# Kernel optimization log

Measured on AMD Instinct MI355X. Metric: run time of the kernel, lower is better.

The kernel has to match this reference:

```python
import jax, jax.numpy as jnp
import numpy as np

B, D, NT, H, K = 4096, 112, 200, 512, 10
HID = 512
IN = 3 * D + NT + 1   # GRU input size = 537
M0 = H + 3 * D + NT   # MLP first-layer input = 1048


def setup_inputs() -> dict:
    key = jax.random.key(0)
    ks = jax.random.split(key, 9)
    def w(k, shape, fan):
        return jax.random.normal(k, shape, jnp.float32) / np.sqrt(fan).astype(np.float32)
    return {
        "z": jax.random.normal(ks[0], (B, D), jnp.float32),
        "c": jax.random.normal(ks[1], (B, D + NT), jnp.float32),
        "b": jax.random.uniform(ks[2], (B, D), jnp.float32),
        "m": jax.random.uniform(ks[3], (B, D), jnp.float32),
        "Wih": w(ks[4], (IN, 3 * H), IN),
        "Whh": w(ks[5], (H, 3 * H), H),
        "bih": jnp.zeros((3 * H,), jnp.float32),
        "bhh": jnp.zeros((3 * H,), jnp.float32),
        "W0": w(ks[6], (M0, HID), M0),
        "b0": jnp.zeros((HID,), jnp.float32),
        "W1": w(ks[7], (HID, HID), HID),
        "b1": jnp.zeros((HID,), jnp.float32),
        "W2": w(ks[8], (HID, 3 * K), HID),
        "b2": jnp.zeros((3 * K,), jnp.float32),
    }


def reference(z, c, b, m, Wih, Whh, bih, bhh, W0, b0, W1, b1, W2, b2):
    """AutoReg.logp: autoregressive GRU + MLP mixture-density head, gaussian base."""
    Bn = z.shape[0]
    const = jnp.concatenate([c, b, m], axis=1)          # [B, 3D+NT] fixed per step
    gi_const = const @ Wih[1:] + bih                    # input-proj of constant part
    w_z = Wih[0]                                        # [3H] weight for scalar z_t
    mlp_const = const @ W0[H:] + b0                     # const part of first MLP layer
    W0h = W0[:H]
    # teacher-forced previous-z sequence: z_0 = -1, then z[:, t-1]
    z_prev = jnp.concatenate([-jnp.ones((Bn, 1), z.dtype), z[:, :-1]], axis=1).T  # [D, B]

    def step(h, zt):  # h: [B,H], zt: [B]
        gi = zt[:, None] * w_z + gi_const               # [B, 3H]
        gh = h @ Whh + bhh
        ir, iz, inn = jnp.split(gi, 3, axis=1)
        hr, hz, hn = jnp.split(gh, 3, axis=1)
        r = jax.nn.sigmoid(ir + hr)
        u = jax.nn.sigmoid(iz + hz)
        n = jnp.tanh(inn + r * hn)
        h2 = (1.0 - u) * n + u * h                      # torch GRU update
        a = jnp.tanh(h2 @ W0h + mlp_const)              # Linear + Tanh on [h||c||b||m]
        a = jnp.tanh(a @ W1 + b1)
        p = a @ W2 + b2                                 # [B, 3K] mixture params
        return h2, p

    h0 = jnp.zeros((Bn, H), z.dtype)
    _, ps = jax.lax.scan(step, h0, z_prev)              # ps: [D, B, 3K]
    params = jnp.transpose(ps, (1, 0, 2))               # [B, D, 3K]

    logits, means, lsig = jnp.split(params, 3, axis=-1)
    sig = jnp.exp(lsig)
    t = z[..., None]
    log_norm = -lsig - 0.5 * np.float32(np.log(2.0 * np.pi))
    log_kern = -0.5 * jnp.square((t - means) / sig)
    ll = jax.nn.logsumexp(log_kern + log_norm + logits, axis=-1) \
         - jax.nn.logsumexp(logits, axis=-1)            # [B, D]

    query = m * (1.0 - b)
    mask = -jnp.sort(-query, axis=1)                    # descending sort values
    return jnp.sum(ll * mask, axis=1)                   # [B]
```

## Files before the change

kernel.cpp:

```cpp
#include <hip/hip_runtime.h>
#include <hip/hip_bf16.h>
#include <float.h>
#include <math.h>

#define BN   4096
#define DD   112
#define HH   512
#define G3   1536
#define CW   536
#define CWP  544
#define HIDD 512

typedef __attribute__((ext_vector_type(8))) short short8;
typedef __attribute__((ext_vector_type(4))) float float4v;

__device__ __forceinline__ unsigned short f2bf(float x) {
    __hip_bfloat16 h = __float2bfloat16(x);
    return *(unsigned short*)&h;
}
__device__ __forceinline__ unsigned char f2fp8(float x) {
    int v = __builtin_amdgcn_cvt_pk_fp8_f32(x, x, 0, false);
    return (unsigned char)(v & 0xff);
}

__global__ void build_constbf(const float* __restrict__ c, const float* __restrict__ b,
                              const float* __restrict__ m, unsigned short* __restrict__ out) {
    int idx = blockIdx.x * blockDim.x + threadIdx.x;
    if (idx >= BN * CWP) return;
    int row = idx / CWP, col = idx - row * CWP;
    float v;
    if (col < 312)      v = c[row * 312 + col];
    else if (col < 424) v = b[row * 112 + (col - 312)];
    else if (col < 536) v = m[row * 112 + (col - 424)];
    else                v = 0.0f;
    out[idx] = f2bf(v);
}

__global__ void zero_f32(float* __restrict__ p, int n) {
    int i = blockIdx.x * blockDim.x + threadIdx.x;
    if (i < n) p[i] = 0.0f;
}

__global__ void pack_wN(const float* __restrict__ src, unsigned short* __restrict__ dst,
                        int kchunks, int ldn, int ncols, int nrows) {
    int bid = blockIdx.x;
    int nt = bid / kchunks, kc = bid - nt * kchunks;
    int lane = threadIdx.x;
    int quad = lane >> 4, l16 = lane & 15;
    int n = nt * 16 + l16;
    unsigned short v[8];
#pragma unroll
    for (int j = 0; j < 8; ++j) {
        int k = kc * 32 + quad * 8 + j;
        float f = (k < nrows && n < ncols) ? src[(size_t)k * ldn + n] : 0.0f;
        v[j] = f2bf(f);
    }
    unsigned short* p = dst + ((size_t)bid * 64 + lane) * 8;
#pragma unroll
    for (int j = 0; j < 8; ++j) p[j] = v[j];
}

__global__ void pack_w8(const float* __restrict__ src, unsigned char* __restrict__ dst,
                        int kchunks, int ldn) {
    int bid = blockIdx.x;
    int nt = bid / kchunks, kc = bid - nt * kchunks;
    int lane = threadIdx.x;
    int quad = lane >> 4, l16 = lane & 15;
    int n = nt * 16 + l16;
    unsigned char v[8];
#pragma unroll
    for (int j = 0; j < 8; ++j) {
        int k = kc * 32 + quad * 8 + j;
        v[j] = f2fp8(src[(size_t)k * ldn + n]);
    }
    unsigned char* p = dst + ((size_t)bid * 64 + lane) * 8;
#pragma unroll
    for (int j = 0; j < 8; ++j) p[j] = v[j];
}

template<int TPW>
__global__ __launch_bounds__(1024) void gemm_const_mfma(
    const unsigned short* __restrict__ A, const unsigned short* __restrict__ BP,
    const float* __restrict__ bias, float* __restrict__ C, int N)
{
    const int tid = threadIdx.x;
    const int wave = tid >> 6, lane = tid & 63;
    const int quad = lane >> 4, l16 = lane & 15;
    const int rowBase = blockIdx.x * 16;
    const short8* BF = (const short8*)BP;
    float4v acc[TPW];
#pragma unroll
    for (int i = 0; i < TPW; ++i) {
        float bv = bias[(wave + 16 * i) * 16 + l16];
        acc[i] = (float4v){bv, bv, bv, bv};
    }
#pragma unroll 4
    for (int kc = 0; kc < 17; ++kc) {
        short8 af = *(const short8*)&A[(size_t)(rowBase + l16) * CWP + kc * 32 + quad * 8];
#pragma unroll
        for (int i = 0; i < TPW; ++i) {
            int tile = wave + 16 * i;
            acc[i] = __builtin_amdgcn_mfma_f32_16x16x32_bf16(af, BF[(tile * 17 + kc) * 64 + lane], acc[i], 0, 0, 0);
        }
    }
#pragma unroll
    for (int i = 0; i < TPW; ++i) {
        int col = (wave + 16 * i) * 16 + l16;
#pragma unroll
        for (int rg = 0; rg < 4; ++rg)
            C[(size_t)(rowBase + quad * 4 + rg) * N + col] = acc[i][rg];
    }
}

__global__ void sort_mask(const float* __restrict__ b, const float* __restrict__ m,
                          float* __restrict__ maskbuf) {
    __shared__ float s[128];
    const int row = blockIdx.x, t = threadIdx.x;
    float v = -FLT_MAX;
    if (t < DD) v = m[row * DD + t] * (1.0f - b[row * DD + t]);
    s[t] = v;
    __syncthreads();
    for (int k = 2; k <= 128; k <<= 1) {
        for (int j = k >> 1; j > 0; j >>= 1) {
            int ixj = t ^ j;
            if (ixj > t) {
                bool up = ((t & k) == 0);
                float a = s[t], bb = s[ixj];
                if ((a > bb) == up) { s[t] = bb; s[ixj] = a; }
            }
            __syncthreads();
        }
    }
    if (t < DD) maskbuf[row * DD + t] = s[127 - t];
}

__global__ __launch_bounds__(1024, 4) void gru_rec_chunk(
    const float* __restrict__ z, const float* __restrict__ Wih,
    const float* __restrict__ bhh, const float* __restrict__ gi_const,
    const unsigned short* __restrict__ WhhP, const unsigned char* __restrict__ Whh8P,
    float* __restrict__ hstate, unsigned short* __restrict__ h2g,
    int t0, int tlen)
{
    __shared__ unsigned short h_bf[2][16 * 520];
    __shared__ unsigned char h8[2][16 * 528];
    __shared__ float zbuf[113 * 16];

    const int tid = threadIdx.x;
    const int wave = tid >> 6, lane = tid & 63;
    const int quad = lane >> 4, l16 = lane & 15;
    const int rowBase = blockIdx.x * 16;

    for (int idx = tid; idx < 113 * 16; idx += 1024) {
        int tt = idx >> 4, r = idx & 15;
        zbuf[idx] = (tt == 0) ? -1.0f : z[(rowBase + r) * DD + tt - 1];
    }

    int hcol[2];
    float wz0[2], wz1[2], wz2[2], bh2r[2];
    float gic0[2][4], gic1[2][4], gic2[2][4];
    float h_own[2][4];
#pragma unroll
    for (int i = 0; i < 2; ++i) {
        int tile = wave + 16 * i;
        int hc = tile * 16 + l16;
        hcol[i] = hc;
        wz0[i] = Wih[hc]; wz1[i] = Wih[512 + hc]; wz2[i] = Wih[1024 + hc];
        float bh0 = bhh[hc], bh1 = bhh[512 + hc];
        bh2r[i] = bhh[1024 + hc];
#pragma unroll
        for (int rg = 0; rg < 4; ++rg) {
            int m = quad * 4 + rg;
            const float* g = gi_const + (size_t)(rowBase + m) * G3;
            gic0[i][rg] = g[hc] + bh0;
            gic1[i][rg] = g[512 + hc] + bh1;
            gic2[i][rg] = g[1024 + hc];
            float hv = hstate[(size_t)(rowBase + m) * HH + hc];
            h_own[i][rg] = hv;
            h_bf[0][m * 520 + hc] = f2bf(hv);
            h8[0][m * 528 + hc] = f2fp8(hv);
        }
    }
    const short8* WhhF = (const short8*)WhhP;
    const long* WhhF8 = (const long*)Whh8P;
    __syncthreads();

    for (int tt = 0; tt < tlen; ++tt) {
        const int t = t0 + tt;
        const int p = tt & 1;
        const unsigned short* hsrc = h_bf[p];
        const unsigned char* h8src = h8[p];
        unsigned short* hdst = h_bf[p ^ 1];
        unsigned char* h8dst = h8[p ^ 1];
        float4v accR[2], accU[2], accN[2];
#pragma unroll
        for (int i = 0; i < 2; ++i) {
            accR[i] = (float4v){gic0[i][0], gic0[i][1], gic0[i][2], gic0[i][3]};
            accU[i] = (float4v){gic1[i][0], gic1[i][1], gic1[i][2], gic1[i][3]};
            accN[i] = (float4v){0.f, 0.f, 0.f, 0.f};
        }
#pragma unroll 8
        for (int kc = 0; kc < 16; ++kc) {
            short8 af = *(const short8*)&hsrc[l16 * 520 + kc * 32 + quad * 8];
            long af8 = *(const long*)&h8src[l16 * 528 + kc * 32 + quad * 8];
#pragma unroll
            for (int i = 0; i < 2; ++i) {
                int tile = wave + 16 * i;
                accR[i] = __builtin_amdgcn_mfma_f32_16x16x32_fp8_fp8(af8, WhhF8[(tile * 16 + kc) * 64 + lane], accR[i], 0, 0, 0);
                accU[i] = __builtin_amdgcn_mfma_f32_16x16x32_fp8_fp8(af8, WhhF8[((tile + 32) * 16 + kc) * 64 + lane], accU[i], 0, 0, 0);
                accN[i] = __builtin_amdgcn_mfma_f32_16x16x32_bf16(af, WhhF[((tile + 64) * 16 + kc) * 64 + lane], accN[i], 0, 0, 0);
            }
        }
#pragma unroll
        for (int i = 0; i < 2; ++i) {
#pragma unroll
            for (int rg = 0; rg < 4; ++rg) {
                int m = quad * 4 + rg;
                float zt = zbuf[t * 16 + m];
                float r = 1.0f / (1.0f + __expf(-(accR[i][rg] + zt * wz0[i])));
                float u = 1.0f / (1.0f + __expf(-(accU[i][rg] + zt * wz1[i])));
                float xn = gic2[i][rg] + zt * wz2[i] + r * (accN[i][rg] + bh2r[i]);
                float n = 1.0f - 2.0f / (__expf(2.0f * xn) + 1.0f);
                float h2 = (1.0f - u) * n + u * h_own[i][rg];
                h_own[i][rg] = h2;
                hdst[m * 520 + hcol[i]] = f2bf(h2);
                h8dst[m * 528 + hcol[i]] = f2fp8(h2);
            }
        }
        __syncthreads();
        {
            int col = lane * 8;
            uint4 v = *(const uint4*)&hdst[wave * 520 + col];
            *(uint4*)&h2g[((size_t)tt * BN + rowBase + wave) * 512 + col] = v;
        }
    }
#pragma unroll
    for (int i = 0; i < 2; ++i)
#pragma unroll
        for (int rg = 0; rg < 4; ++rg)
            hstate[(size_t)(rowBase + quad * 4 + rg) * HH + hcol[i]] = h_own[i][rg];
}

__global__ __launch_bounds__(1024) void head_mdn64(
    const float* __restrict__ z, const float* __restrict__ b1,
    const float* __restrict__ b2, const float* __restrict__ mlp_const,
    const float* __restrict__ maskbuf, const unsigned short* __restrict__ h2g,
    const unsigned short* __restrict__ W0hP, const unsigned short* __restrict__ W1P,
    const unsigned short* __restrict__ W2P, float* __restrict__ out, int t0)
{
    __shared__ unsigned short h_bf[64 * 520];
    __shared__ unsigned short a_bf[64 * 520];
    float* ppf = (float*)a_bf;

    const int tid = threadIdx.x;
    const int wave = tid >> 6, lane = tid & 63;
    const int quad = lane >> 4, l16 = lane & 15;
    const int pr = tid >> 5, pc = tid & 31;
    const int b0 = blockIdx.x * 4;
    const int tg = blockIdx.y;
    const int phase = blockIdx.x & 15;

    {
        int flat = tid * 32;
        int r = flat >> 9, col = flat & 511;
        int bb = b0 + (r >> 4), trel = tg * 16 + (r & 15);
        const uint4* src = (const uint4*)&h2g[((size_t)trel * BN + bb) * 512 + col];
        uint4 v0 = src[0], v1 = src[1], v2 = src[2], v3 = src[3];
        uint4* dst = (uint4*)&h_bf[r * 520 + col];
        dst[0] = v0; dst[1] = v1; dst[2] = v2; dst[3] = v3;
    }
    int hcol[2];
    float b1c[2], mlc[2][4];
#pragma unroll
    for (int i = 0; i < 2; ++i) {
        int hc = (wave + 16 * i) * 16 + l16;
        hcol[i] = hc;
        b1c[i] = b1[hc];
#pragma unroll
        for (int mt = 0; mt < 4; ++mt) mlc[i][mt] = mlp_const[(size_t)(b0 + mt) * HIDD + hc];
    }
    const float b2v = (pc < 30) ? b2[pc] : 0.0f;
    const short8* W0hF = (const short8*)W0hP;
    const short8* W1F  = (const short8*)W1P;
    const short8* W2F  = (const short8*)W2P;
    __syncthreads();

    float4v acc1[2][4];
#pragma unroll
    for (int i = 0; i < 2; ++i)
#pragma unroll
        for (int mt = 0; mt < 4; ++mt)
            acc1[i][mt] = (float4v){mlc[i][mt], mlc[i][mt], mlc[i][mt], mlc[i][mt]};
#pragma unroll 2
    for (int kk = 0; kk < 16; ++kk) {
        const int kc = (kk + phase) & 15;
        short8 af[4];
#pragma unroll
        for (int mt = 0; mt < 4; ++mt)
            af[mt] = *(const short8*)&h_bf[(mt * 16 + l16) * 520 + kc * 32 + quad * 8];
#pragma unroll
        for (int i = 0; i < 2; ++i) {
            short8 bf = W0hF[((wave + 16 * i) * 16 + kc) * 64 + lane];
#pragma unroll
            for (int mt = 0; mt < 4; ++mt)
                acc1[i][mt] = __builtin_amdgcn_mfma_f32_16x16x32_bf16(af[mt], bf, acc1[i][mt], 0, 0, 0);
        }
    }
#pragma unroll
    for (int i = 0; i < 2; ++i)
#pragma unroll
        for (int mt = 0; mt < 4; ++mt)
#pragma unroll
            for (int rg = 0; rg < 4; ++rg) {
                int m = mt * 16 + quad * 4 + rg;
                float x = acc1[i][mt][rg];
                a_bf[m * 520 + hcol[i]] = f2bf(1.0f - 2.0f / (__expf(2.0f * x) + 1.0f));
            }
    __syncthreads();
    float4v acc2[2][4];
#pragma unroll
    for (int i = 0; i < 2; ++i)
#pragma unroll
        for (int mt = 0; mt < 4; ++mt)
            acc2[i][mt] = (float4v){b1c[i], b1c[i], b1c[i], b1c[i]};
#pragma unroll 2
    for (int kk = 0; kk < 16; ++kk) {
        const int kc = (kk + phase) & 15;
        short8 af[4];
#pragma unroll
        for (int mt = 0; mt < 4; ++mt)
            af[mt] = *(const short8*)&a_bf[(mt * 16 + l16) * 520 + kc * 32 + quad * 8];
#pragma unroll
        for (int i = 0; i < 2; ++i) {
            short8 bf = W1F[((wave + 16 * i) * 16 + kc) * 64 + lane];
#pragma unroll
            for (int mt = 0; mt < 4; ++mt)
                acc2[i][mt] = __builtin_amdgcn_mfma_f32_16x16x32_bf16(af[mt], bf, acc2[i][mt], 0, 0, 0);
        }
    }
    __syncthreads();
#pragma unroll
    for (int i = 0; i < 2; ++i)
#pragma unroll
        for (int mt = 0; mt < 4; ++mt)
#pragma unroll
            for (int rg = 0; rg < 4; ++rg) {
                int m = mt * 16 + quad * 4 + rg;
                float x = acc2[i][mt][rg];
                h_bf[m * 520 + hcol[i]] = f2bf(1.0f - 2.0f / (__expf(2.0f * x) + 1.0f));
            }
    __syncthreads();
    {
        const int mtw = wave >> 2, kg = wave & 3;
        float4v ap0 = (float4v){0.f, 0.f, 0.f, 0.f}, ap1 = (float4v){0.f, 0.f, 0.f, 0.f};
#pragma unroll
        for (int kk = 0; kk < 4; ++kk) {
            int kc = kg * 4 + kk;
            short8 af = *(const short8*)&h_bf[(mtw * 16 + l16) * 520 + kc * 32 + quad * 8];
            ap0 = __builtin_amdgcn_mfma_f32_16x16x32_bf16(af, W2F[(0 * 16 + kc) * 64 + lane], ap0, 0, 0, 0);
            ap1 = __builtin_amdgcn_mfma_f32_16x16x32_bf16(af, W2F[(1 * 16 + kc) * 64 + lane], ap1, 0, 0, 0);
        }
#pragma unroll
        for (int rg = 0; rg < 4; ++rg) {
            ppf[((kg * 4 + mtw) * 2 + 0) * 256 + lane * 4 + rg] = ap0[rg];
            ppf[((kg * 4 + mtw) * 2 + 1) * 256 + lane * 4 + rg] = ap1[rg];
        }
    }
    __syncthreads();
    float llm[2];
#pragma unroll
    for (int rh = 0; rh < 2; ++rh) {
        const int slot = rh * 32 + pr;
        const int bsub = slot >> 4, toff = slot & 15;
        const int mm = slot & 15;
        const int lane_c = ((mm >> 2) * 16 + (pc & 15));
        const int rgc = mm & 3, ntv = pc >> 4;
        float pv = b2v;
#pragma unroll
        for (int kg = 0; kg < 4; ++kg)
            pv += ppf[((kg * 4 + bsub) * 2 + ntv) * 256 + lane_c * 4 + rgc];
        const int half = lane & 32;
        float meanv = __shfl(pv, half + ((pc + 10) & 31), 64);
        float lsigv = __shfl(pv, half + ((pc + 20) & 31), 64);
        float e1, e2;
        if (pc < 10) {
            float ztar = z[(size_t)(b0 + bsub) * DD + t0 + tg * 16 + toff];
            float invs = __expf(-lsigv);
            float dd = (ztar - meanv) * invs;
            e1 = -0.5f * dd * dd - lsigv - 0.91893853320467274f + pv;
            e2 = pv;
        } else { e1 = -FLT_MAX; e2 = -FLT_MAX; }
        float m1 = e1, m2 = e2;
#pragma unroll
        for (int off = 16; off > 0; off >>= 1) {
            m1 = fmaxf(m1, __shfl_xor(m1, off, 64));
            m2 = fmaxf(m2, __shfl_xor(m2, off, 64));
        }
        float s1 = (pc < 10) ? __expf(e1 - m1) : 0.0f;
        float s2 = (pc < 10) ? __expf(e2 - m2) : 0.0f;
#pragma unroll
        for (int off = 16; off > 0; off >>= 1) {
            s1 += __shfl_xor(s1, off, 64);
            s2 += __shfl_xor(s2, off, 64);
        }
        float ll = (m1 + __logf(s1)) - (m2 + __logf(s2));
        llm[rh] = ll * maskbuf[(size_t)(b0 + bsub) * DD + t0 + tg * 16 + toff];
    }
    __syncthreads();
    if (pc == 0) { ppf[pr] = llm[0]; ppf[32 + pr] = llm[1]; }
    __syncthreads();
    if (tid < 4) {
        float s = 0.0f;
#pragma unroll
        for (int j = 0; j < 16; ++j) s += ppf[tid * 16 + j];
        atomicAdd(&out[b0 + tid], s);
    }
}

extern "C" void kernel_launch(void* const* d_in, const int* in_sizes, int n_in,
                              void* d_out, int out_size, void* d_ws, size_t ws_size,
                              hipStream_t stream) {
    const float* z   = (const float*)d_in[0];
    const float* c   = (const float*)d_in[1];
    const float* b   = (const float*)d_in[2];
    const float* m   = (const float*)d_in[3];
    const float* Wih = (const float*)d_in[4];
    const float* Whh = (const float*)d_in[5];
    const float* bih = (const float*)d_in[6];
    const float* bhh = (const float*)d_in[7];
    const float* W0  = (const float*)d_in[8];
    const float* b0  = (const float*)d_in[9];
    const float* W1  = (const float*)d_in[10];
    const float* b1  = (const float*)d_in[11];
    const float* W2  = (const float*)d_in[12];
    const float* b2  = (const float*)d_in[13];
    float* out = (float*)d_out;

    char* p = (char*)d_ws;
    unsigned short* constbf = (unsigned short*)p;  p += (size_t)BN * CWP * 2;
    float* gi_const  = (float*)p;                  p += (size_t)BN * G3 * 4;
    float* mlp_const = (float*)p;                  p += (size_t)BN * HIDD * 4;
    float* maskbuf   = (float*)p;                  p += (size_t)BN * DD * 4;
    unsigned short* WihP = (unsigned short*)p;     p += (size_t)96 * 17 * 512 * 2;
    unsigned short* W0cP = (unsigned short*)p;     p += (size_t)32 * 17 * 512 * 2;
    unsigned short* WhhP = (unsigned short*)p;     p += (size_t)96 * 16 * 512 * 2;
    unsigned short* W0hP = (unsigned short*)p;     p += (size_t)32 * 16 * 512 * 2;
    unsigned short* W1P  = (unsigned short*)p;     p += (size_t)32 * 16 * 512 * 2;
    unsigned short* W2P  = (unsigned short*)p;     p += (size_t)2 * 16 * 512 * 2;
    unsigned char* Whh8P = (unsigned char*)p;      p += (size_t)64 * 16 * 512;
    float* hstate        = (float*)p;              p += (size_t)BN * HH * 4;
    unsigned short* h2g  = (unsigned short*)p;

    const size_t base = (size_t)(p - (char*)d_ws);
    const size_t slab_per_t = (size_t)BN * 512 * 2;
    int TC = 0;
    if (ws_size > base) {
        TC = (int)((ws_size - base) / slab_per_t);
        TC = (TC / 16) * 16;
        if (TC > DD) TC = DD;
    }
    if (TC < 16) return;

    build_constbf<<<(BN * CWP + 255) / 256, 256, 0, stream>>>(c, b, m, constbf);
    pack_wN<<<96 * 17, 64, 0, stream>>>(Wih + G3, WihP, 17, G3, G3, CW);
    pack_wN<<<32 * 17, 64, 0, stream>>>(W0 + (size_t)HH * HIDD, W0cP, 17, HIDD, HIDD, CW);
    pack_wN<<<96 * 16, 64, 0, stream>>>(Whh, WhhP, 16, G3, G3, HH);
    pack_w8<<<64 * 16, 64, 0, stream>>>(Whh, Whh8P, 16, G3);
    pack_wN<<<32 * 16, 64, 0, stream>>>(W0,  W0hP, 16, HIDD, HIDD, HH);
    pack_wN<<<32 * 16, 64, 0, stream>>>(W1,  W1P,  16, HIDD, HIDD, HH);
    pack_wN<<<2 * 16, 64, 0, stream>>>(W2,  W2P,  16, 30, 30, HH);
    gemm_const_mfma<6><<<BN / 16, 1024, 0, stream>>>(constbf, WihP, bih, gi_const, G3);
    gemm_const_mfma<2><<<BN / 16, 1024, 0, stream>>>(constbf, W0cP, b0, mlp_const, HIDD);
    sort_mask<<<BN, 128, 0, stream>>>(b, m, maskbuf);

    zero_f32<<<(BN * HH + 255) / 256, 256, 0, stream>>>(hstate, BN * HH);
    zero_f32<<<(BN + 255) / 256, 256, 0, stream>>>(out, BN);
    for (int t0 = 0; t0 < DD; t0 += TC) {
        int tlen = DD - t0 < TC ? DD - t0 : TC;
        gru_rec_chunk<<<BN / 16, 1024, 0, stream>>>(z, Wih, bhh, gi_const, WhhP, Whh8P,
                                                    hstate, h2g, t0, tlen);
        dim3 gh(BN / 4, tlen / 16);
        head_mdn64<<<gh, 1024, 0, stream>>>(z, b1, b2, mlp_const, maskbuf, h2g,
                                            W0hP, W1P, W2P, out, t0);
    }
}
```

Measured before the change: 2.760 ms.

## Use FP8 for the GRU n-gate recurrent matmul and pair K-chunks into 16-byte loads

```diff
diff --git a/kernel.cpp b/kernel.cpp
--- a/kernel.cpp
+++ b/kernel.cpp
@@ -13,6 +13,7 @@
 
 typedef __attribute__((ext_vector_type(8))) short short8;
 typedef __attribute__((ext_vector_type(4))) float float4v;
+typedef __attribute__((ext_vector_type(2))) long long2v;
 
 __device__ __forceinline__ unsigned short f2bf(float x) {
     __hip_bfloat16 h = __float2bfloat16(x);
@@ -60,22 +61,22 @@
     for (int j = 0; j < 8; ++j) p[j] = v[j];
 }
 
-__global__ void pack_w8(const float* __restrict__ src, unsigned char* __restrict__ dst,
-                        int kchunks, int ldn) {
+__global__ void pack_w8p(const float* __restrict__ src, unsigned char* __restrict__ dst,
+                         int ldn) {
     int bid = blockIdx.x;
-    int nt = bid / kchunks, kc = bid - nt * kchunks;
+    int nt = bid >> 3, kp = bid & 7;
     int lane = threadIdx.x;
     int quad = lane >> 4, l16 = lane & 15;
     int n = nt * 16 + l16;
-    unsigned char v[8];
-#pragma unroll
-    for (int j = 0; j < 8; ++j) {
-        int k = kc * 32 + quad * 8 + j;
-        v[j] = f2fp8(src[(size_t)k * ldn + n]);
-    }
-    unsigned char* p = dst + ((size_t)bid * 64 + lane) * 8;
-#pragma unroll
-    for (int j = 0; j < 8; ++j) p[j] = v[j];
+    unsigned char v[16];
+#pragma unroll
+    for (int j2 = 0; j2 < 16; ++j2) {
+        int k = kp * 64 + (j2 >> 3) * 32 + quad * 8 + (j2 & 7);
+        v[j2] = f2fp8(src[(size_t)k * ldn + n]);
+    }
+    unsigned char* p = dst + ((size_t)bid * 64 + lane) * 16;
+#pragma unroll
+    for (int j2 = 0; j2 < 16; ++j2) p[j2] = v[j2];
 }
 
 template<int TPW>
@@ -137,7 +138,7 @@
 __global__ __launch_bounds__(1024, 4) void gru_rec_chunk(
     const float* __restrict__ z, const float* __restrict__ Wih,
     const float* __restrict__ bhh, const float* __restrict__ gi_const,
-    const unsigned short* __restrict__ WhhP, const unsigned char* __restrict__ Whh8P,
+    const unsigned char* __restrict__ Whh8P,
     float* __restrict__ hstate, unsigned short* __restrict__ h2g,
     int t0, int tlen)
 {
@@ -155,7 +156,7 @@
         zbuf[idx] = (tt == 0) ? -1.0f : z[(rowBase + r) * DD + tt - 1];
     }
 
-    int hcol[2];
+    int hcol[2], h8off[2];
     float wz0[2], wz1[2], wz2[2], bh2r[2];
     float gic0[2][4], gic1[2][4], gic2[2][4];
     float h_own[2][4];
@@ -164,6 +165,10 @@
         int tile = wave + 16 * i;
         int hc = tile * 16 + l16;
         hcol[i] = hc;
+        {
+            int kp = hc >> 6, rem = hc & 63;
+            h8off[i] = kp * 64 + ((rem & 31) >> 3) * 16 + (rem >> 5) * 8 + (rem & 7);
+        }
         wz0[i] = Wih[hc]; wz1[i] = Wih[512 + hc]; wz2[i] = Wih[1024 + hc];
         float bh0 = bhh[hc], bh1 = bhh[512 + hc];
         bh2r[i] = bhh[1024 + hc];
@@ -177,17 +182,15 @@
             float hv = hstate[(size_t)(rowBase + m) * HH + hc];
             h_own[i][rg] = hv;
             h_bf[0][m * 520 + hc] = f2bf(hv);
-            h8[0][m * 528 + hc] = f2fp8(hv);
-        }
-    }
-    const short8* WhhF = (const short8*)WhhP;
-    const long* WhhF8 = (const long*)Whh8P;
+            h8[0][m * 528 + h8off[i]] = f2fp8(hv);
+        }
+    }
+    const long2v* W8F = (const long2v*)Whh8P;
     __syncthreads();
 
     for (int tt = 0; tt < tlen; ++tt) {
         const int t = t0 + tt;
         const int p = tt & 1;
-        const unsigned short* hsrc = h_bf[p];
         const unsigned char* h8src = h8[p];
         unsigned short* hdst = h_bf[p ^ 1];
         unsigned char* h8dst = h8[p ^ 1];
@@ -199,15 +202,20 @@
             accN[i] = (float4v){0.f, 0.f, 0.f, 0.f};
         }
 #pragma unroll 8
-        for (int kc = 0; kc < 16; ++kc) {
-            short8 af = *(const short8*)&hsrc[l16 * 520 + kc * 32 + quad * 8];
-            long af8 = *(const long*)&h8src[l16 * 528 + kc * 32 + quad * 8];
+        for (int kp = 0; kp < 8; ++kp) {
+            long2v afp = *(const long2v*)&h8src[l16 * 528 + kp * 64 + quad * 16];
 #pragma unroll
             for (int i = 0; i < 2; ++i) {
                 int tile = wave + 16 * i;
-                accR[i] = __builtin_amdgcn_mfma_f32_16x16x32_fp8_fp8(af8, WhhF8[(tile * 16 + kc) * 64 + lane], accR[i], 0, 0, 0);
-                accU[i] = __builtin_amdgcn_mfma_f32_16x16x32_fp8_fp8(af8, WhhF8[((tile + 32) * 16 + kc) * 64 + lane], accU[i], 0, 0, 0);
-                accN[i] = __builtin_amdgcn_mfma_f32_16x16x32_bf16(af, WhhF[((tile + 64) * 16 + kc) * 64 + lane], accN[i], 0, 0, 0);
+                long2v wR = W8F[((tile) * 8 + kp) * 64 + lane];
+                long2v wU = W8F[((tile + 32) * 8 + kp) * 64 + lane];
+                long2v wN = W8F[((tile + 64) * 8 + kp) * 64 + lane];
+                accR[i] = __builtin_amdgcn_mfma_f32_16x16x32_fp8_fp8(afp.x, wR.x, accR[i], 0, 0, 0);
+                accR[i] = __builtin_amdgcn_mfma_f32_16x16x32_fp8_fp8(afp.y, wR.y, accR[i], 0, 0, 0);
+                accU[i] = __builtin_amdgcn_mfma_f32_16x16x32_fp8_fp8(afp.x, wU.x, accU[i], 0, 0, 0);
+                accU[i] = __builtin_amdgcn_mfma_f32_16x16x32_fp8_fp8(afp.y, wU.y, accU[i], 0, 0, 0);
+                accN[i] = __builtin_amdgcn_mfma_f32_16x16x32_fp8_fp8(afp.x, wN.x, accN[i], 0, 0, 0);
+                accN[i] = __builtin_amdgcn_mfma_f32_16x16x32_fp8_fp8(afp.y, wN.y, accN[i], 0, 0, 0);
             }
         }
 #pragma unroll
@@ -223,7 +231,7 @@
                 float h2 = (1.0f - u) * n + u * h_own[i][rg];
                 h_own[i][rg] = h2;
                 hdst[m * 520 + hcol[i]] = f2bf(h2);
-                h8dst[m * 528 + hcol[i]] = f2fp8(h2);
+                h8dst[m * 528 + h8off[i]] = f2fp8(h2);
             }
         }
         __syncthreads();
@@ -442,11 +450,10 @@
     float* maskbuf   = (float*)p;                  p += (size_t)BN * DD * 4;
     unsigned short* WihP = (unsigned short*)p;     p += (size_t)96 * 17 * 512 * 2;
     unsigned short* W0cP = (unsigned short*)p;     p += (size_t)32 * 17 * 512 * 2;
-    unsigned short* WhhP = (unsigned short*)p;     p += (size_t)96 * 16 * 512 * 2;
     unsigned short* W0hP = (unsigned short*)p;     p += (size_t)32 * 16 * 512 * 2;
     unsigned short* W1P  = (unsigned short*)p;     p += (size_t)32 * 16 * 512 * 2;
     unsigned short* W2P  = (unsigned short*)p;     p += (size_t)2 * 16 * 512 * 2;
-    unsigned char* Whh8P = (unsigned char*)p;      p += (size_t)64 * 16 * 512;
+    unsigned char* Whh8P = (unsigned char*)p;      p += (size_t)96 * 8 * 64 * 16;
     float* hstate        = (float*)p;              p += (size_t)BN * HH * 4;
     unsigned short* h2g  = (unsigned short*)p;
 
@@ -463,8 +470,7 @@
     build_constbf<<<(BN * CWP + 255) / 256, 256, 0, stream>>>(c, b, m, constbf);
     pack_wN<<<96 * 17, 64, 0, stream>>>(Wih + G3, WihP, 17, G3, G3, CW);
     pack_wN<<<32 * 17, 64, 0, stream>>>(W0 + (size_t)HH * HIDD, W0cP, 17, HIDD, HIDD, CW);
-    pack_wN<<<96 * 16, 64, 0, stream>>>(Whh, WhhP, 16, G3, G3, HH);
-    pack_w8<<<64 * 16, 64, 0, stream>>>(Whh, Whh8P, 16, G3);
+    pack_w8p<<<96 * 8, 64, 0, stream>>>(Whh, Whh8P, G3);
     pack_wN<<<32 * 16, 64, 0, stream>>>(W0,  W0hP, 16, HIDD, HIDD, HH);
     pack_wN<<<32 * 16, 64, 0, stream>>>(W1,  W1P,  16, HIDD, HIDD, HH);
     pack_wN<<<2 * 16, 64, 0, stream>>>(W2,  W2P,  16, 30, 30, HH);
@@ -476,7 +482,7 @@
     zero_f32<<<(BN + 255) / 256, 256, 0, stream>>>(out, BN);
     for (int t0 = 0; t0 < DD; t0 += TC) {
         int tlen = DD - t0 < TC ? DD - t0 : TC;
-        gru_rec_chunk<<<BN / 16, 1024, 0, stream>>>(z, Wih, bhh, gi_const, WhhP, Whh8P,
+        gru_rec_chunk<<<BN / 16, 1024, 0, stream>>>(z, Wih, bhh, gi_const, Whh8P,
                                                     hstate, h2g, t0, tlen);
         dim3 gh(BN / 4, tlen / 16);
         head_mdn64<<<gh, 1024, 0, stream>>>(z, b1, b2, mlp_const, maskbuf, h2g,
```

After: 3.841 ms. +39.2%, slower.
